# Performance work log

Measured on AMD Instinct MI355X. Metric: run time of the kernel, lower is better.

The kernel has to match this reference:

```python
import jax, jax.numpy as jnp
import numpy as np

# dims: T tokens, E experts, D model dim, F ffn dim, C per-expert capacity, K top-k routing
T, E, D, F, C, K = 4096, 8, 1024, 4096, 1536, 2


def setup_inputs() -> dict:
    key = jax.random.key(0)
    k_x, k_lg, k_w1, k_w2 = jax.random.split(key, 4)
    x = jax.random.normal(k_x, (T, D), jnp.float32)
    # external router: top-K of logits per token, softmax weights over kept logits
    logits = jax.random.normal(k_lg, (T, E), jnp.float32)
    topv, topi = jax.lax.top_k(logits, K)                      # (T,K)
    rows = jnp.arange(T)[:, None]
    route_mask = jnp.zeros((T, E), bool).at[rows, topi].set(True)
    route_weight = jnp.zeros((T, E), jnp.float32).at[rows, topi].set(
        jax.nn.softmax(topv, axis=-1))
    # stacked homogeneous expert MLP params (E leading axis, as in _stack_group)
    W1 = jax.random.normal(k_w1, (E, D, F), jnp.float32) / np.sqrt(D)
    b1 = jnp.zeros((E, F), jnp.float32)
    W2 = jax.random.normal(k_w2, (E, F, D), jnp.float32) / np.sqrt(F)
    b2 = jnp.zeros((E, D), jnp.float32)
    return dict(x=x, route_mask=route_mask, route_weight=route_weight,
                W1=W1, b1=b1, W2=W2, b2=b2)


def reference(x, route_mask, route_weight, W1, b1, W2, b2):
    """MoE with per-expert capacity: top-C tokens per expert by route weight,
    gather -> vmapped expert MLP -> weighted scatter-combine.
    Math identical to the one-hot slot einsums ('ect,t...->ec...' dispatch and
    'ecf,ect,te->tf' combine) of the original, expressed as gather/scatter.
    """
    Tn, En = route_mask.shape
    w_te = jnp.where(route_mask, route_weight, 0.0)            # (T,E)
    # per-expert scores; unrouted tokens get -inf so they can never be selected
    w_et = jnp.where(route_mask.T, w_te.T, -jnp.inf)           # (E,T)
    vals, idx = jax.lax.top_k(w_et, C)                         # (E,C) token ids per slot
    valid = jnp.isfinite(vals)                                  # slot actually filled
    # dispatch: gather token features into (E,C,D); empty slots are zero rows
    xe = x[idx] * valid[..., None]
    # grouped expert MLP (vmap over E via batched einsum)
    h = jax.nn.relu(jnp.einsum('ecd,edf->ecf', xe, W1) + b1[:, None, :])
    out = jnp.einsum('ecf,efd->ecd', h, W2) + b2[:, None, :]    # (E,C,D)
    # combine: y[t] = sum over slots assigned to t of w_te[t,e] * out[e,c]
    gain = jnp.where(valid, jnp.take_along_axis(w_te.T, idx, axis=1), 0.0)  # (E,C)
    y = jnp.zeros((Tn, out.shape[-1]), out.dtype)
    y = y.at[idx.reshape(-1)].add((out * gain[..., None]).reshape(-1, out.shape[-1]))
    return y
```

## Files before the change

### kernel.cpp

```cpp
#include <hip/hip_runtime.h>
#include <hip/hip_bf16.h>
#include <stdint.h>

#define T_TOK 4096
#define NE    8
#define DM    1024
#define FF    4096
#define CAP   1536

typedef __attribute__((ext_vector_type(8))) __bf16 bf16x8;
typedef __attribute__((ext_vector_type(4))) float  f32x4;

__device__ __forceinline__ void gload_lds16(const void* gptr, void* lptr) {
  __builtin_amdgcn_global_load_lds(
      (__attribute__((address_space(1))) void*)(uintptr_t)gptr,
      (__attribute__((address_space(3))) void*)(uintptr_t)lptr,
      16, 0, 0);
}


__global__ void conv_x_kernel(const float4* __restrict__ src, ushort4* __restrict__ dst, int n4) {
  int i = blockIdx.x * blockDim.x + threadIdx.x;
  if (i >= n4) return;
  float4 v = src[i];
  ushort4 o;
  o.x = __builtin_bit_cast(unsigned short, __float2bfloat16(v.x));
  o.y = __builtin_bit_cast(unsigned short, __float2bfloat16(v.y));
  o.z = __builtin_bit_cast(unsigned short, __float2bfloat16(v.z));
  o.w = __builtin_bit_cast(unsigned short, __float2bfloat16(v.w));
  dst[i] = o;
}

__global__ __launch_bounds__(256)
void tconv_kernel(const float* __restrict__ src, __hip_bfloat16* __restrict__ dst,
                  int R, int C) {
  __shared__ float tile[64][65];
  const int b  = blockIdx.z;
  const int r0 = blockIdx.y * 64;
  const int c0 = blockIdx.x * 64;
  const float* s = src + (size_t)b * R * C;
  __hip_bfloat16* d = dst + (size_t)b * R * C;
  const int tid = threadIdx.x;
  const int tx = tid & 63, ty = tid >> 6;
#pragma unroll
  for (int rr = ty; rr < 64; rr += 4)
    tile[rr][tx] = s[(size_t)(r0 + rr) * C + c0 + tx];
  __syncthreads();
  const int lg = tid & 15;
  const int cg = tid >> 4;
#pragma unroll
  for (int w = 0; w < 4; ++w) {
    const int cc = w * 16 + cg;
    const int r4 = lg * 4;
    ushort4 o;
    o.x = __builtin_bit_cast(unsigned short, __float2bfloat16(tile[r4 + 0][cc]));
    o.y = __builtin_bit_cast(unsigned short, __float2bfloat16(tile[r4 + 1][cc]));
    o.z = __builtin_bit_cast(unsigned short, __float2bfloat16(tile[r4 + 2][cc]));
    o.w = __builtin_bit_cast(unsigned short, __float2bfloat16(tile[r4 + 3][cc]));
    *(ushort4*)&d[(size_t)(c0 + cc) * R + r0 + r4] = o;
  }
}

__global__ void router_kernel(const float* __restrict__ rw, int* __restrict__ counts,
                              int* __restrict__ tok_ids, float* __restrict__ gains) {
  int t = blockIdx.x * blockDim.x + threadIdx.x;
  if (t >= T_TOK) return;
#pragma unroll
  for (int e = 0; e < NE; ++e) {
    float w = rw[t * NE + e];
    if (w > 0.f) {
      int pos = atomicAdd(&counts[e], 1);
      if (pos < CAP) {
        tok_ids[e * CAP + pos] = t;
        gains[e * CAP + pos]   = w;
      }
    }
  }
}

__global__ void pad_kernel(const int* __restrict__ counts, int* __restrict__ tok_ids,
                           float* __restrict__ gains) {
  int i = blockIdx.x * blockDim.x + threadIdx.x;
  if (i >= NE * CAP) return;
  int e = i / CAP, pos = i % CAP;
  int ne = min(counts[e], CAP);
  if (pos >= ne) { tok_ids[i] = 0; gains[i] = 0.f; }
}


template <int PASS, int SK>
__global__ __launch_bounds__(256, 4)
void moe_gemm97(const __hip_bfloat16* __restrict__ Asrc,
                const __hip_bfloat16* __restrict__ Bsrc,
                const float* __restrict__ bias,
                const int* __restrict__ counts,
                const int* __restrict__ tok_ids,
                const float* __restrict__ gains,
                __hip_bfloat16* __restrict__ Hout,
                float* __restrict__ y)
{
  constexpr int K   = (PASS == 1) ? DM : FF;
  constexpr int NP  = (PASS == 1) ? FF : DM;
  constexpr int MT  = CAP / 128;
  constexpr int NT  = NP / 128;
  constexpr int KP  = K / SK;
  constexpr int KT  = KP / 32;
  constexpr int NWG = NE * MT * NT * SK;

  const int id = (blockIdx.x & 7) * (NWG / 8) + (blockIdx.x >> 3);
  const int e  = id / (SK * NT * MT);
  int r        = id % (SK * NT * MT);
  const int sp = r / (NT * MT);
  r            = r % (NT * MT);
  const int nt = r / MT;
  const int mt = r % MT;

  const int Ne = min(counts[e], CAP);
  const int m0 = mt * 128;
  if (m0 >= Ne) return;
  const int n0 = nt * 128;
  const int k0 = sp * KP;

  __shared__ alignas(16) __hip_bfloat16 As[128 * 32];
  __shared__ alignas(16) __hip_bfloat16 Bs[128 * 32];

  const int tid  = threadIdx.x;
  const int lane = tid & 63;
  const int wid  = tid >> 6;
  const int wm   = wid >> 1;
  const int wn   = wid & 1;

  const int srow = tid >> 2;
  const int cs   = ((tid & 3) ^ ((srow >> 1) & 3)) * 8;

  const __hip_bfloat16 *aptr0, *aptr1;
  if (PASS == 1) {
    const int tok0 = tok_ids[e * CAP + m0 + srow];
    const int tok1 = tok_ids[e * CAP + m0 + 64 + srow];
    aptr0 = Asrc + (size_t)tok0 * DM + k0 + cs;
    aptr1 = Asrc + (size_t)tok1 * DM + k0 + cs;
  } else {
    aptr0 = Asrc + ((size_t)e * CAP + m0 + srow) * FF + k0 + cs;
    aptr1 = Asrc + ((size_t)e * CAP + m0 + 64 + srow) * FF + k0 + cs;
  }
  const __hip_bfloat16* bptr0 = Bsrc + (((size_t)e * NP + n0 + srow) * K) + k0 + cs;
  const __hip_bfloat16* bptr1 = Bsrc + (((size_t)e * NP + n0 + 64 + srow) * K) + k0 + cs;

  const char* AsB = (const char*)As;
  const char* BsB = (const char*)Bs;
  const int fr = lane & 15;
  const int fq = lane >> 4;
  const int kbyte = ((fq ^ ((fr >> 1) & 3)) << 4);

  f32x4 acc[4][4] = {};

  for (int kt = 0; kt < KT; ++kt) {
    gload_lds16(aptr0 + kt * 32, (char*)As + wid * 1024);
    gload_lds16(aptr1 + kt * 32, (char*)As + 4096 + wid * 1024);
    gload_lds16(bptr0 + kt * 32, (char*)Bs + wid * 1024);
    gload_lds16(bptr1 + kt * 32, (char*)Bs + 4096 + wid * 1024);
    __syncthreads();

    bf16x8 af[4], bfr[4];
#pragma unroll
    for (int i = 0; i < 4; ++i)
      af[i] = *(const bf16x8*)(AsB + (wm * 64 + i * 16 + fr) * 64 + kbyte);
#pragma unroll
    for (int j = 0; j < 4; ++j)
      bfr[j] = *(const bf16x8*)(BsB + (wn * 64 + j * 16 + fr) * 64 + kbyte);
#pragma unroll
    for (int i = 0; i < 4; ++i)
#pragma unroll
      for (int j = 0; j < 4; ++j)
        acc[i][j] = __builtin_amdgcn_mfma_f32_16x16x32_bf16(af[i], bfr[j], acc[i][j], 0, 0, 0);
    __syncthreads();
  }

  const int colb = n0 + wn * 64 + fr;
  if (PASS == 1) {
#pragma unroll
    for (int j = 0; j < 4; ++j) {
      const float bv = bias[(size_t)e * NP + colb + j * 16];
#pragma unroll
      for (int i = 0; i < 4; ++i)
#pragma unroll
        for (int rr = 0; rr < 4; ++rr) {
          const int row = m0 + wm * 64 + i * 16 + fq * 4 + rr;
          float v = acc[i][j][rr] + bv;
          v = v > 0.f ? v : 0.f;
          Hout[((size_t)e * CAP + row) * FF + colb + j * 16] = __float2bfloat16(v);
        }
    }
  } else {
    float bv[4];
#pragma unroll
    for (int j = 0; j < 4; ++j)
      bv[j] = (sp == 0) ? bias[(size_t)e * NP + colb + j * 16] : 0.f;
#pragma unroll
    for (int i = 0; i < 4; ++i)
#pragma unroll
      for (int rr = 0; rr < 4; ++rr) {
        const int row  = m0 + wm * 64 + i * 16 + fq * 4 + rr;
        const int slot = e * CAP + row;
        const float g  = gains[slot];
        if (g != 0.f) {
          const int tok = tok_ids[slot];
          float* yrow = y + (size_t)tok * DM + colb;
#pragma unroll
          for (int j = 0; j < 4; ++j)
            atomicAdd(yrow + j * 16, (acc[i][j][rr] + bv[j]) * g);
        }
      }
  }
}


extern "C" void kernel_launch(void* const* d_in, const int* in_sizes, int n_in,
                              void* d_out, int out_size, void* d_ws, size_t ws_size,
                              hipStream_t stream) {
  const float* x  = (const float*)d_in[0];
  const float* rw = (const float*)d_in[2];
  const float* W1 = (const float*)d_in[3];
  const float* b1 = (const float*)d_in[4];
  const float* W2 = (const float*)d_in[5];
  const float* b2 = (const float*)d_in[6];
  float* y = (float*)d_out;

  char* ws = (char*)d_ws;
  size_t off = 0;
  auto alloc = [&](size_t bytes) {
    void* p = ws + off;
    off = (off + bytes + 255) & ~(size_t)255;
    return p;
  };
  __hip_bfloat16* xb  = (__hip_bfloat16*)alloc((size_t)T_TOK * DM * 2);
  __hip_bfloat16* w1t = (__hip_bfloat16*)alloc((size_t)NE * DM * FF * 2);
  __hip_bfloat16* w2t = (__hip_bfloat16*)alloc((size_t)NE * FF * DM * 2);
  __hip_bfloat16* Hb  = (__hip_bfloat16*)alloc((size_t)NE * CAP * FF * 2);
  int*   counts  = (int*)alloc(NE * sizeof(int));
  int*   tok_ids = (int*)alloc((size_t)NE * CAP * sizeof(int));
  float* gains   = (float*)alloc((size_t)NE * CAP * sizeof(float));
  (void)ws_size; (void)in_sizes; (void)n_in; (void)out_size;

  hipMemsetAsync(y, 0, (size_t)T_TOK * DM * sizeof(float), stream);
  hipMemsetAsync(counts, 0, NE * sizeof(int), stream);

  conv_x_kernel<<<(T_TOK * DM / 4 + 255) / 256, 256, 0, stream>>>(
      (const float4*)x, (ushort4*)xb, T_TOK * DM / 4);
  tconv_kernel<<<dim3(FF / 64, DM / 64, NE), 256, 0, stream>>>(W1, w1t, DM, FF);
  tconv_kernel<<<dim3(DM / 64, FF / 64, NE), 256, 0, stream>>>(W2, w2t, FF, DM);
  router_kernel<<<(T_TOK + 255) / 256, 256, 0, stream>>>(rw, counts, tok_ids, gains);
  pad_kernel<<<(NE * CAP + 255) / 256, 256, 0, stream>>>(counts, tok_ids, gains);

  moe_gemm97<1, 1><<<NE * (CAP / 128) * (FF / 128) * 1, 256, 0, stream>>>(
      xb, w1t, b1, counts, tok_ids, gains, Hb, nullptr);
  moe_gemm97<2, 4><<<NE * (CAP / 128) * (DM / 128) * 4, 256, 0, stream>>>(
      Hb, w2t, b2, counts, tok_ids, gains, nullptr, y);
}
```

Baseline: 388.4 us.

## Widen GEMM K-tile to 64, drop split-K, and remove XCD-aware block remap

The MoE GEMM kernel now stages a 64-wide K slice per iteration instead of 32, with a new 8-chunk XOR swizzle, so there are half as many barriers per unit of work. The second GEMM drops its 4-way split-K and launches a quarter as many workgroups, each covering the full K. That removes three quarters of the atomic adds into y but leaves only 8*12*8 blocks, which may underfill the GPU. The block-id remap that spread consecutive blocks across XCDs is also removed, and occupancy bounds drop from 4 to 2 waves per SIMD hint.

```diff
diff --git a/kernel.cpp b/kernel.cpp
--- a/kernel.cpp
+++ b/kernel.cpp
@@ -88,41 +88,36 @@
 }
 
 
-template <int PASS, int SK>
-__global__ __launch_bounds__(256, 4)
-void moe_gemm97(const __hip_bfloat16* __restrict__ Asrc,
-                const __hip_bfloat16* __restrict__ Bsrc,
-                const float* __restrict__ bias,
-                const int* __restrict__ counts,
-                const int* __restrict__ tok_ids,
-                const float* __restrict__ gains,
-                __hip_bfloat16* __restrict__ Hout,
-                float* __restrict__ y)
+template <int PASS>
+__global__ __launch_bounds__(256, 2)
+void moe_gemm(const __hip_bfloat16* __restrict__ Asrc,
+              const __hip_bfloat16* __restrict__ Bsrc,
+              const float* __restrict__ bias,
+              const int* __restrict__ counts,
+              const int* __restrict__ tok_ids,
+              const float* __restrict__ gains,
+              __hip_bfloat16* __restrict__ Hout,
+              float* __restrict__ y)
 {
-  constexpr int K   = (PASS == 1) ? DM : FF;
-  constexpr int NP  = (PASS == 1) ? FF : DM;
-  constexpr int MT  = CAP / 128;
-  constexpr int NT  = NP / 128;
-  constexpr int KP  = K / SK;
-  constexpr int KT  = KP / 32;
-  constexpr int NWG = NE * MT * NT * SK;
-
-  const int id = (blockIdx.x & 7) * (NWG / 8) + (blockIdx.x >> 3);
-  const int e  = id / (SK * NT * MT);
-  int r        = id % (SK * NT * MT);
-  const int sp = r / (NT * MT);
-  r            = r % (NT * MT);
-  const int nt = r / MT;
-  const int mt = r % MT;
+  constexpr int K  = (PASS == 1) ? DM : FF;
+  constexpr int NP = (PASS == 1) ? FF : DM;
+  constexpr int MT = CAP / 128;
+  constexpr int NT = NP / 128;
+  constexpr int KT = K / 64;
+
+  const int bid = blockIdx.x;
+  const int e   = bid / (MT * NT);
+  const int rem = bid % (MT * NT);
+  const int mt  = rem / NT;
+  const int nt  = rem % NT;
 
   const int Ne = min(counts[e], CAP);
   const int m0 = mt * 128;
   if (m0 >= Ne) return;
   const int n0 = nt * 128;
-  const int k0 = sp * KP;
-
-  __shared__ alignas(16) __hip_bfloat16 As[128 * 32];
-  __shared__ alignas(16) __hip_bfloat16 Bs[128 * 32];
+
+  __shared__ alignas(16) __hip_bfloat16 As[128 * 64];
+  __shared__ alignas(16) __hip_bfloat16 Bs[128 * 64];
 
   const int tid  = threadIdx.x;
   const int lane = tid & 63;
@@ -130,49 +125,56 @@
   const int wm   = wid >> 1;
   const int wn   = wid & 1;
 
-  const int srow = tid >> 2;
-  const int cs   = ((tid & 3) ^ ((srow >> 1) & 3)) * 8;
-
-  const __hip_bfloat16 *aptr0, *aptr1;
-  if (PASS == 1) {
-    const int tok0 = tok_ids[e * CAP + m0 + srow];
-    const int tok1 = tok_ids[e * CAP + m0 + 64 + srow];
-    aptr0 = Asrc + (size_t)tok0 * DM + k0 + cs;
-    aptr1 = Asrc + (size_t)tok1 * DM + k0 + cs;
-  } else {
-    aptr0 = Asrc + ((size_t)e * CAP + m0 + srow) * FF + k0 + cs;
-    aptr1 = Asrc + ((size_t)e * CAP + m0 + 64 + srow) * FF + k0 + cs;
-  }
-  const __hip_bfloat16* bptr0 = Bsrc + (((size_t)e * NP + n0 + srow) * K) + k0 + cs;
-  const __hip_bfloat16* bptr1 = Bsrc + (((size_t)e * NP + n0 + 64 + srow) * K) + k0 + cs;
+  const int srow8 = (tid >> 3) & 7;
+  const int cs    = ((tid & 7) ^ srow8) * 8;
+
+  const __hip_bfloat16 *aP[4], *bP[4];
+#pragma unroll
+  for (int i = 0; i < 4; ++i) {
+    const int row = i * 32 + (tid >> 3);
+    if (PASS == 1) {
+      const int tok = tok_ids[e * CAP + m0 + row];
+      aP[i] = Asrc + (size_t)tok * DM + cs;
+    } else {
+      aP[i] = Asrc + ((size_t)e * CAP + m0 + row) * FF + cs;
+    }
+    bP[i] = Bsrc + ((size_t)e * NP + n0 + row) * K + cs;
+  }
 
   const char* AsB = (const char*)As;
   const char* BsB = (const char*)Bs;
   const int fr = lane & 15;
   const int fq = lane >> 4;
-  const int kbyte = ((fq ^ ((fr >> 1) & 3)) << 4);
+  const int kb0 = ((fq + 0) ^ (fr & 7)) << 4;
+  const int kb1 = ((fq + 4) ^ (fr & 7)) << 4;
 
   f32x4 acc[4][4] = {};
 
   for (int kt = 0; kt < KT; ++kt) {
-    gload_lds16(aptr0 + kt * 32, (char*)As + wid * 1024);
-    gload_lds16(aptr1 + kt * 32, (char*)As + 4096 + wid * 1024);
-    gload_lds16(bptr0 + kt * 32, (char*)Bs + wid * 1024);
-    gload_lds16(bptr1 + kt * 32, (char*)Bs + 4096 + wid * 1024);
+#pragma unroll
+    for (int i = 0; i < 4; ++i)
+      gload_lds16(aP[i] + kt * 64, (char*)As + i * 4096 + tid * 16);
+#pragma unroll
+    for (int i = 0; i < 4; ++i)
+      gload_lds16(bP[i] + kt * 64, (char*)Bs + i * 4096 + tid * 16);
     __syncthreads();
 
-    bf16x8 af[4], bfr[4];
-#pragma unroll
-    for (int i = 0; i < 4; ++i)
-      af[i] = *(const bf16x8*)(AsB + (wm * 64 + i * 16 + fr) * 64 + kbyte);
-#pragma unroll
-    for (int j = 0; j < 4; ++j)
-      bfr[j] = *(const bf16x8*)(BsB + (wn * 64 + j * 16 + fr) * 64 + kbyte);
-#pragma unroll
-    for (int i = 0; i < 4; ++i)
+#pragma unroll
+    for (int s = 0; s < 2; ++s) {
+      const int kb = s ? kb1 : kb0;
+      bf16x8 af[4], bfr[4];
+#pragma unroll
+      for (int i = 0; i < 4; ++i)
+        af[i] = *(const bf16x8*)(AsB + (wm * 64 + i * 16 + fr) * 128 + kb);
 #pragma unroll
       for (int j = 0; j < 4; ++j)
-        acc[i][j] = __builtin_amdgcn_mfma_f32_16x16x32_bf16(af[i], bfr[j], acc[i][j], 0, 0, 0);
+        bfr[j] = *(const bf16x8*)(BsB + (wn * 64 + j * 16 + fr) * 128 + kb);
+#pragma unroll
+      for (int i = 0; i < 4; ++i)
+#pragma unroll
+        for (int j = 0; j < 4; ++j)
+          acc[i][j] = __builtin_amdgcn_mfma_f32_16x16x32_bf16(af[i], bfr[j], acc[i][j], 0, 0, 0);
+    }
     __syncthreads();
   }
 
@@ -194,8 +196,7 @@
   } else {
     float bv[4];
 #pragma unroll
-    for (int j = 0; j < 4; ++j)
-      bv[j] = (sp == 0) ? bias[(size_t)e * NP + colb + j * 16] : 0.f;
+    for (int j = 0; j < 4; ++j) bv[j] = bias[(size_t)e * NP + colb + j * 16];
 #pragma unroll
     for (int i = 0; i < 4; ++i)
 #pragma unroll
@@ -252,8 +253,8 @@
   router_kernel<<<(T_TOK + 255) / 256, 256, 0, stream>>>(rw, counts, tok_ids, gains);
   pad_kernel<<<(NE * CAP + 255) / 256, 256, 0, stream>>>(counts, tok_ids, gains);
 
-  moe_gemm97<1, 1><<<NE * (CAP / 128) * (FF / 128) * 1, 256, 0, stream>>>(
+  moe_gemm<1><<<NE * (CAP / 128) * (FF / 128), 256, 0, stream>>>(
       xb, w1t, b1, counts, tok_ids, gains, Hb, nullptr);
-  moe_gemm97<2, 4><<<NE * (CAP / 128) * (DM / 128) * 4, 256, 0, stream>>>(
+  moe_gemm<2><<<NE * (CAP / 128) * (DM / 128), 256, 0, stream>>>(
       Hb, w2t, b2, counts, tok_ids, gains, nullptr, y);
 }
```

Result: faster. 323.7 us (-16.7%).
